# Optimization experiments

Measured on AMD Instinct MI355X. Metric: run time of the kernel, lower is better.

The kernel has to match this reference:

```python
import jax, jax.numpy as jnp
import numpy as np

B, S, D, H, N = 2, 2048, 768, 12, 128  # batch, seq_len, d_model, n_heads, num_segments
EPS_LN = 1e-5


def _layer_norm(x, g, b):
    m = x.mean(-1, keepdims=True)
    v = ((x - m) ** 2).mean(-1, keepdims=True)
    return (x - m) / jnp.sqrt(v + EPS_LN) * g + b


def _mha(q, k, v, Wqkv, bqkv, Wo, bo, n_heads):
    """torch.nn.MultiheadAttention (batch_first), returns (out, head-averaged attn)."""
    d = q.shape[-1]
    dh = d // n_heads
    Wq, Wk, Wv = jnp.split(Wqkv, 3, axis=0)
    bq, bk, bv = jnp.split(bqkv, 3)
    qh = (q @ Wq.T + bq).reshape(q.shape[0], q.shape[1], n_heads, dh)
    kh = (k @ Wk.T + bk).reshape(k.shape[0], k.shape[1], n_heads, dh)
    vh = (v @ Wv.T + bv).reshape(v.shape[0], v.shape[1], n_heads, dh)
    scores = jnp.einsum('bqhd,bkhd->bhqk', qh, kh) / jnp.sqrt(jnp.asarray(dh, q.dtype))
    attn = jax.nn.softmax(scores, axis=-1)                      # [B,H,Sq,Sk]
    out = jnp.einsum('bhqk,bkhd->bqhd', attn, vh).reshape(q.shape[0], q.shape[1], d)
    return out @ Wo.T + bo, attn.mean(axis=1)                   # attn avg over heads


def _aggregate(x, w, seg):  # per-batch: weighted mean of tokens into N segments
    num = jax.ops.segment_sum(w[:, None] * x, seg, num_segments=N)
    den = jax.ops.segment_sum(w, seg, num_segments=N)
    return num / (den[:, None] + 1e-8)


def setup_inputs() -> dict:
    key = jax.random.key(0)
    ks = jax.random.split(key, 16)
    s = 0.02
    inp = {
        'hidden_states': jax.random.normal(ks[0], (B, S, D), jnp.float32),
        'token_to_segment': jnp.sort(jax.random.randint(ks[1], (B, S), 0, N), axis=-1),
        # token_attention (shared for node-level self-attn in the adjacency=None branch)
        'Wqkv_t': jax.random.normal(ks[2], (3 * D, D), jnp.float32) * s,
        'bqkv_t': jnp.zeros((3 * D,), jnp.float32),
        'Wo_t': jax.random.normal(ks[3], (D, D), jnp.float32) * s,
        'bo_t': jnp.zeros((D,), jnp.float32),
        # cross_attention
        'Wqkv_c': jax.random.normal(ks[4], (3 * D, D), jnp.float32) * s,
        'bqkv_c': jnp.zeros((3 * D,), jnp.float32),
        'Wo_c': jax.random.normal(ks[5], (D, D), jnp.float32) * s,
        'bo_c': jnp.zeros((D,), jnp.float32),
        # layer norms
        'g_tok': jnp.ones((D,), jnp.float32),
        'b_tok': jnp.zeros((D,), jnp.float32),
        'g_node': jnp.ones((D,), jnp.float32),
        'b_node': jnp.zeros((D,), jnp.float32),
        # output projection
        'W_out': jax.random.normal(ks[6], (D, D), jnp.float32) * s,
        'b_out': jnp.zeros((D,), jnp.float32),
    }
    return inp


def reference(hidden_states, token_to_segment, Wqkv_t, bqkv_t, Wo_t, bo_t,
              Wqkv_c, bqkv_c, Wo_c, bo_c, g_tok, b_tok, g_node, b_node,
              W_out, b_out):
    hs = hidden_states
    # token-level self-attention + residual norm
    tok_attn_out, tok_attn = _mha(hs, hs, hs, Wqkv_t, bqkv_t, Wo_t, bo_t, H)
    token_output = _layer_norm(hs + tok_attn_out, g_tok, b_tok)
    # token -> node attention-weighted scatter aggregation
    w = tok_attn.mean(axis=1)  # [B,S] attention received per token
    node_emb = jax.vmap(_aggregate)(token_output, w, token_to_segment)  # [B,N,D]
    # node-level self-attention (reuses token_attention weights; adjacency=None path)
    node_out, node_attn = _mha(node_emb, node_emb, node_emb, Wqkv_t, bqkv_t, Wo_t, bo_t, H)
    node_emb = _layer_norm(node_emb + node_out, g_node, b_node)
    # cross-attention: tokens attend to nodes
    cross_out, cross_w = _mha(token_output, node_emb, node_emb, Wqkv_c, bqkv_c, Wo_c, bo_c, H)
    token_output = token_output + cross_out
    # node -> token gather + additive combine
    gathered = jnp.take_along_axis(node_emb, token_to_segment[:, :, None], axis=1)  # [B,S,D]
    enhanced = token_output + gathered
    output = enhanced @ W_out.T + b_out
    return output, node_emb, tok_attn, node_attn, cross_w
```

## Files before the change

### kernel.cpp

```cpp
#include <hip/hip_runtime.h>
#include <cstdint>

#define B_ 2
#define S_ 2048
#define D_ 768
#define H_ 12
#define DH_ 64
#define N_ 128

typedef unsigned short u16;
typedef unsigned int u32;
typedef unsigned long long u64;
typedef __attribute__((ext_vector_type(8))) short short8;
typedef __attribute__((ext_vector_type(4))) float f32x4;

#define MFMA16(a, b, c) __builtin_amdgcn_mfma_f32_16x16x32_bf16(a, b, c, 0, 0, 0)

__device__ inline u16 f2bf(float f) {
  union { float f; u32 u; } v; v.f = f;
  u32 r = v.u + 0x7FFFu + ((v.u >> 16) & 1u);
  return (u16)(r >> 16);
}
__device__ inline u32 pk2(float a, float b) {
  return (u32)f2bf(a) | ((u32)f2bf(b) << 16);
}
__device__ inline float bf2f(u16 h) {
  union { u32 u; float f; } v; v.u = ((u32)h) << 16;
  return v.f;
}
__device__ inline float wredmax(float v) {
  #pragma unroll
  for (int o = 32; o > 0; o >>= 1) v = fmaxf(v, __shfl_down(v, o));
  return v;
}
__device__ inline float wredsum(float v) {
  #pragma unroll
  for (int o = 32; o > 0; o >>= 1) v += __shfl_down(v, o);
  return v;
}
__device__ inline void async_lds16(const u16* g, u16* l) {
  __builtin_amdgcn_global_load_lds((const __attribute__((address_space(1))) void*)g,
                                   (__attribute__((address_space(3))) void*)l, 16, 0, 0);
}

__global__ void conv_bf16(const float* __restrict__ in, u16* __restrict__ outp, int n8) {
  int i = blockIdx.x * 256 + threadIdx.x;
  if (i >= n8) return;
  const float4* p = (const float4*)(in + (size_t)i * 8);
  float4 a = p[0], b = p[1];
  uint4 u;
  u.x = pk2(a.x, a.y); u.y = pk2(a.z, a.w); u.z = pk2(b.x, b.y); u.w = pk2(b.z, b.w);
  *(uint4*)(outp + (size_t)i * 8) = u;
}

template <int OUT_BF16>
__global__ __launch_bounds__(256) void gemm_bf16(
    const u16* __restrict__ A, int lda,
    const u16* __restrict__ W, int ldb,
    const float* __restrict__ bias,
    void* __restrict__ Cout, int ldc, int K) {
  __shared__ u16 As[128 * 32];
  __shared__ u16 Ws[128 * 32];
  const int tid = threadIdx.x;
  const int m0 = blockIdx.y * 128, n0 = blockIdx.x * 128;
  const int w = tid >> 6, lane = tid & 63;
  const int msub = (w & 1) * 64, nsub = (w >> 1) * 64;
  const int lrow = lane & 15, quad = lane >> 4;
  const int e0 = tid * 8;
  const int r0 = e0 >> 5, c0 = e0 & 31;
  const int e1 = e0 + 2048;
  const int r1 = e1 >> 5, c1 = e1 & 31;
  const u16* Ag0 = A + (size_t)(m0 + r0) * lda + c0;
  const u16* Ag1 = A + (size_t)(m0 + r1) * lda + c1;
  const u16* Wg0 = W + (size_t)(n0 + r0) * ldb + c0;
  const u16* Wg1 = W + (size_t)(n0 + r1) * ldb + c1;
  u16* AsB0 = As + (w << 9);
  u16* AsB1 = As + 2048 + (w << 9);
  u16* WsB0 = Ws + (w << 9);
  u16* WsB1 = Ws + 2048 + (w << 9);
  f32x4 zero = {0.f, 0.f, 0.f, 0.f};
  f32x4 acc[4][4];
  #pragma unroll
  for (int i = 0; i < 4; i++)
    #pragma unroll
    for (int j = 0; j < 4; j++) acc[i][j] = zero;
  for (int k0 = 0; k0 < K; k0 += 32) {
    __syncthreads();
    async_lds16(Ag0 + k0, AsB0);
    async_lds16(Ag1 + k0, AsB1);
    async_lds16(Wg0 + k0, WsB0);
    async_lds16(Wg1 + k0, WsB1);
    __syncthreads();
    short8 af[4], bf[4];
    #pragma unroll
    for (int i = 0; i < 4; i++)
      af[i] = *(const short8*)(As + (msub + i * 16 + lrow) * 32 + quad * 8);
    #pragma unroll
    for (int j = 0; j < 4; j++)
      bf[j] = *(const short8*)(Ws + (nsub + j * 16 + lrow) * 32 + quad * 8);
    #pragma unroll
    for (int i = 0; i < 4; i++)
      #pragma unroll
      for (int j = 0; j < 4; j++)
        acc[i][j] = MFMA16(af[i], bf[j], acc[i][j]);
  }
  #pragma unroll
  for (int i = 0; i < 4; i++) {
    #pragma unroll
    for (int j = 0; j < 4; j++) {
      int col = n0 + nsub + j * 16 + lrow;
      float bv = bias ? bias[col] : 0.f;
      #pragma unroll
      for (int r = 0; r < 4; r++) {
        int row = m0 + msub + i * 16 + quad * 4 + r;
        float val = acc[i][j][r] + bv;
        if (OUT_BF16) ((u16*)Cout)[(size_t)row * ldc + col] = f2bf(val);
        else ((float*)Cout)[(size_t)row * ldc + col] = val;
      }
    }
  }
}

__global__ __launch_bounds__(256) void transpose_v(const u16* __restrict__ qkv, u16* __restrict__ VT) {
  __shared__ u16 t[64][72];
  const int z = blockIdx.y, b = z / 12, h = z - b * 12;
  const int s0 = blockIdx.x * 64;
  const int tid = threadIdx.x;
  {
    int r = tid >> 2, dp = (tid & 3) * 16;
    const u16* src = qkv + (size_t)b * 2048 * 2304 + (size_t)(s0 + r) * 2304 + 1536 + h * 64 + dp;
    *(uint4*)&t[r][dp] = *(const uint4*)src;
    *(uint4*)&t[r][dp + 8] = *(const uint4*)(src + 8);
  }
  __syncthreads();
  int d = tid >> 2, sp = (tid & 3) * 16;
  u16 vals[16];
  #pragma unroll
  for (int i = 0; i < 16; i++) vals[i] = t[sp + i][d];
  u16* dst = VT + ((size_t)z * 64 + d) * 2048 + s0 + sp;
  *(uint4*)dst = *(uint4*)&vals[0];
  *(uint4*)(dst + 8) = *(uint4*)&vals[8];
}

__global__ __launch_bounds__(512, 4) void fused_tok_attn(
    const u16* __restrict__ qkv, const u16* __restrict__ VT,
    float* __restrict__ amF, u16* __restrict__ amH, u16* __restrict__ attnout) {
  __shared__ u16 pbuf[8][16][264];
  __shared__ float lred[8][16];
  __shared__ float obuf[2][16][66];
  const int tid = threadIdx.x;
  const int w = tid >> 6, lane = tid & 63;
  const int lrow = lane & 15, quad = lane >> 4;
  const int b = blockIdx.y, q0 = blockIdx.x << 4, z = blockIdx.z;
  const int h0 = z * 6;
  const u16* qp = qkv + (size_t)b * 2048 * 2304;
  const u16* kp = qp + 768;
  const int strip = w * 256;
  const int jj = w & 3, shalf = w >> 2;
  u16* ob = attnout + (size_t)b * 2048 * 768 + (size_t)q0 * 768;
  u16* pb = &pbuf[w][0][0];
  f32x4 zero = {0.f, 0.f, 0.f, 0.f};
  float amreg[8][8];
  #pragma unroll
  for (int c = 0; c < 8; c++)
    #pragma unroll
    for (int e = 0; e < 8; e++) amreg[c][e] = 0.f;
  for (int hh = 0; hh < 6; hh++) {
    const int h = h0 + hh;
    const u16* qh = qp + (size_t)(q0 + lrow) * 2304 + h * 64 + quad * 8;
    short8 qf0 = *(const short8*)qh;
    short8 qf1 = *(const short8*)(qh + 32);
    float lsum = 0.f;
    #pragma unroll
    for (int t = 0; t < 16; t++) {
      const u16* kh = kp + (size_t)(strip + t * 16 + lrow) * 2304 + h * 64 + quad * 8;
      short8 kf0 = *(const short8*)kh;
      short8 kf1 = *(const short8*)(kh + 32);
      f32x4 sv = zero;
      sv = MFMA16(kf0, qf0, sv);
      sv = MFMA16(kf1, qf1, sv);
      float pe0 = __expf(sv[0] * 0.125f);
      float pe1 = __expf(sv[1] * 0.125f);
      float pe2 = __expf(sv[2] * 0.125f);
      float pe3 = __expf(sv[3] * 0.125f);
      lsum += (pe0 + pe1) + (pe2 + pe3);
      u32 w0 = pk2(pe0, pe1), w1 = pk2(pe2, pe3);
      *(u64*)(pb + lrow * 264 + t * 16 + quad * 4) = (u64)w0 | ((u64)w1 << 32);
    }
    lsum += __shfl_xor(lsum, 16);
    lsum += __shfl_xor(lsum, 32);
    if (lane < 16) lred[w][lane] = lsum;
    __syncthreads();
    float invq;
    float inv4[4];
    {
      float s = 0.f;
      #pragma unroll
      for (int w2 = 0; w2 < 8; w2++) s += lred[w2][lrow];
      invq = 1.f / s;
      #pragma unroll
      for (int r = 0; r < 4; r++) {
        float sr = 0.f;
        #pragma unroll
        for (int w2 = 0; w2 < 8; w2++) sr += lred[w2][quad * 4 + r];
        inv4[r] = 1.f / sr;
      }
    }
    #pragma unroll
    for (int c = 0; c < 8; c++) {
      short8 pf = *(const short8*)(pb + lrow * 264 + c * 32 + quad * 8);
      #pragma unroll
      for (int e = 0; e < 8; e++)
        amreg[c][e] += bf2f((u16)pf[e]) * invq;
    }
    f32x4 oacc = zero;
    {
      const u16* vtp = VT + (size_t)(b * 12 + h) * 64 * 2048;
      const u16* vbase = vtp + (size_t)(jj * 16 + lrow) * 2048 + shalf * 1024 + quad * 8;
      const u16* pbase = &pbuf[shalf * 4][lrow][quad * 8];
      #pragma unroll
      for (int cc = 0; cc < 32; cc++) {
        short8 pf = *(const short8*)(pbase + (cc >> 3) * (16 * 264) + (cc & 7) * 32);
        short8 vf = *(const short8*)(vbase + cc * 32);
        oacc = MFMA16(pf, vf, oacc);
      }
    }
    #pragma unroll
    for (int r = 0; r < 4; r++)
      obuf[shalf][quad * 4 + r][jj * 16 + lrow] = oacc[r] * inv4[r];
    __syncthreads();
    #pragma unroll
    for (int ee = 0; ee < 2; ee++) {
      int e2 = tid + ee * 512;
      int row = e2 >> 6, col = e2 & 63;
      float s = obuf[0][row][col] + obuf[1][row][col];
      ob[(size_t)row * 768 + h * 64 + col] = f2bf(s);
    }
  }
  if (z == 0) {
    float* ar = amF + ((size_t)b * 2048 + q0 + lrow) * 2048 + strip;
    #pragma unroll
    for (int c = 0; c < 8; c++) {
      float4 v0 = {amreg[c][0], amreg[c][1], amreg[c][2], amreg[c][3]};
      float4 v1 = {amreg[c][4], amreg[c][5], amreg[c][6], amreg[c][7]};
      *(float4*)(ar + c * 32 + quad * 8) = v0;
      *(float4*)(ar + c * 32 + quad * 8 + 4) = v1;
    }
  } else {
    u16* ar = amH + ((size_t)b * 2048 + q0 + lrow) * 2048 + strip;
    #pragma unroll
    for (int c = 0; c < 8; c++) {
      uint4 u;
      u.x = pk2(amreg[c][0], amreg[c][1]);
      u.y = pk2(amreg[c][2], amreg[c][3]);
      u.z = pk2(amreg[c][4], amreg[c][5]);
      u.w = pk2(amreg[c][6], amreg[c][7]);
      *(uint4*)(ar + c * 32 + quad * 8) = u;
    }
  }
}

__global__ void combine_am(float* __restrict__ amF, const u16* __restrict__ amH) {
  size_t i = ((size_t)blockIdx.x * 256 + threadIdx.x) * 8;
  float4 a0 = *(float4*)(amF + i);
  float4 a1 = *(float4*)(amF + i + 4);
  uint4 hb = *(const uint4*)(amH + i);
  const float c12 = 1.f / 12.f;
  float4 r0, r1;
  r0.x = (a0.x + bf2f((u16)(hb.x & 0xffff))) * c12;
  r0.y = (a0.y + bf2f((u16)(hb.x >> 16))) * c12;
  r0.z = (a0.z + bf2f((u16)(hb.y & 0xffff))) * c12;
  r0.w = (a0.w + bf2f((u16)(hb.y >> 16))) * c12;
  r1.x = (a1.x + bf2f((u16)(hb.z & 0xffff))) * c12;
  r1.y = (a1.y + bf2f((u16)(hb.z >> 16))) * c12;
  r1.z = (a1.z + bf2f((u16)(hb.w & 0xffff))) * c12;
  r1.w = (a1.w + bf2f((u16)(hb.w >> 16))) * c12;
  *(float4*)(amF + i) = r0;
  *(float4*)(amF + i + 4) = r1;
}

__global__ __launch_bounds__(256) void qk_mfma(
    const u16* __restrict__ Q, int ldq, long qbs,
    const u16* __restrict__ Kp, int ldk, long kbs,
    float* __restrict__ S, long szs, int Sk, int nh, float scale) {
  __shared__ u16 Qs[128 * 72];
  __shared__ u16 Ks[128 * 72];
  const int tid = threadIdx.x;
  const int z = blockIdx.z, bb = z / nh, h = z - bb * nh;
  const u16* qp = Q + (size_t)bb * qbs + h * 64;
  const u16* kp = Kp + (size_t)bb * kbs + h * 64;
  float* sp = S + (size_t)z * szs;
  const int m0 = blockIdx.y * 128, n0 = blockIdx.x * 128;
  const int w = tid >> 6, lane = tid & 63;
  const int msub = (w & 1) * 64, nsub = (w >> 1) * 64;
  const int lrow = lane & 15, quad = lane >> 4;
  const int srow = tid >> 1, shalf = tid & 1;
  {
    const uint4* qg = (const uint4*)(qp + (size_t)(m0 + srow) * ldq + shalf * 32);
    const uint4* kg = (const uint4*)(kp + (size_t)(n0 + srow) * ldk + shalf * 32);
    uint4* qd = (uint4*)(Qs + srow * 72 + shalf * 32);
    uint4* kd = (uint4*)(Ks + srow * 72 + shalf * 32);
    #pragma unroll
    for (int u = 0; u < 4; u++) { qd[u] = qg[u]; kd[u] = kg[u]; }
  }
  __syncthreads();
  f32x4 zero = {0.f, 0.f, 0.f, 0.f};
  f32x4 acc[4][4];
  #pragma unroll
  for (int i = 0; i < 4; i++)
    #pragma unroll
    for (int j = 0; j < 4; j++) acc[i][j] = zero;
  #pragma unroll
  for (int ks = 0; ks < 2; ks++) {
    short8 af[4], bf[4];
    #pragma unroll
    for (int i = 0; i < 4; i++)
      af[i] = *(const short8*)(Qs + (msub + i * 16 + lrow) * 72 + ks * 32 + quad * 8);
    #pragma unroll
    for (int j = 0; j < 4; j++)
      bf[j] = *(const short8*)(Ks + (nsub + j * 16 + lrow) * 72 + ks * 32 + quad * 8);
    #pragma unroll
    for (int i = 0; i < 4; i++)
      #pragma unroll
      for (int j = 0; j < 4; j++)
        acc[i][j] = MFMA16(af[i], bf[j], acc[i][j]);
  }
  #pragma unroll
  for (int i = 0; i < 4; i++)
    #pragma unroll
    for (int j = 0; j < 4; j++) {
      int col = n0 + nsub + j * 16 + lrow;
      #pragma unroll
      for (int r = 0; r < 4; r++) {
        int row = m0 + msub + i * 16 + quad * 4 + r;
        sp[(size_t)row * Sk + col] = acc[i][j][r] * scale;
      }
    }
}

__global__ __launch_bounds__(128) void softmax_small(
    float* __restrict__ Sc, float* __restrict__ wout, int Sq) {
  const int q = blockIdx.x, b = blockIdx.y, tid = threadIdx.x;
  const int w = tid >> 6, lane = tid & 63;
  __shared__ float red[2];
  float am = 0.f;
  const size_t plane = (size_t)Sq * 128;
  for (int h = 0; h < 12; h++) {
    const int z = b * 12 + h;
    float* row = Sc + (size_t)z * plane + (size_t)q * 128;
    float v = row[tid];
    float m = wredmax(v);
    if (lane == 0) red[w] = m;
    __syncthreads();
    m = fmaxf(red[0], red[1]);
    float e = __expf(v - m);
    float s = wredsum(e);
    __syncthreads();
    if (lane == 0) red[w] = s;
    __syncthreads();
    float p = e / (red[0] + red[1]);
    ((u16*)(Sc + (size_t)z * plane))[(size_t)q * 256 + tid] = f2bf(p);
    am += p;
    __syncthreads();
  }
  wout[((size_t)b * Sq + q) * 128 + tid] = am * (1.f / 12.f);
}

__global__ __launch_bounds__(256) void pv_small(
    const u16* __restrict__ Pb, long pzs,
    const u16* __restrict__ KVb, int ldv, long vbs, int vhoff,
    u16* __restrict__ Outb, long obs) {
  __shared__ u16 Ps[128 * 40];
  __shared__ u16 Vs[64 * 40];
  const int tid = threadIdx.x;
  const int z = blockIdx.y, b = z / 12, h = z - b * 12;
  const u16* Pp = Pb + (size_t)z * pzs;
  const u16* Vp = KVb + (size_t)b * vbs + vhoff + h * 64;
  u16* Op = Outb + (size_t)b * obs + h * 64;
  const int m0 = blockIdx.x * 128;
  const int w = tid >> 6, lane = tid & 63;
  const int msub = w * 32;
  const int lrow = lane & 15, quad = lane >> 4;
  const int srow = tid >> 1, shalf = tid & 1;
  const int vk = tid >> 3, vn = (tid & 7) * 8;
  f32x4 zero = {0.f, 0.f, 0.f, 0.f};
  f32x4 acc[2][4];
  #pragma unroll
  for (int i = 0; i < 2; i++)
    #pragma unroll
    for (int j = 0; j < 4; j++) acc[i][j] = zero;
  #pragma unroll
  for (int k0 = 0; k0 < 128; k0 += 32) {
    uint4 pa = *(const uint4*)(Pp + (size_t)(m0 + srow) * 256 + k0 + shalf * 16);
    uint4 pb2 = *(const uint4*)(Pp + (size_t)(m0 + srow) * 256 + k0 + shalf * 16 + 8);
    uint4 vv = *(const uint4*)(Vp + (size_t)(k0 + vk) * ldv + vn);
    __syncthreads();
    *(uint4*)(Ps + srow * 40 + shalf * 16) = pa;
    *(uint4*)(Ps + srow * 40 + shalf * 16 + 8) = pb2;
    const u16* vs = (const u16*)&vv;
    #pragma unroll
    for (int u = 0; u < 8; u++) Vs[(vn + u) * 40 + vk] = vs[u];
    __syncthreads();
    short8 af[2], bf[4];
    #pragma unroll
    for (int i = 0; i < 2; i++)
      af[i] = *(const short8*)(Ps + (msub + i * 16 + lrow) * 40 + quad * 8);
    #pragma unroll
    for (int j = 0; j < 4; j++)
      bf[j] = *(const short8*)(Vs + (j * 16 + lrow) * 40 + quad * 8);
    #pragma unroll
    for (int i = 0; i < 2; i++)
      #pragma unroll
      for (int j = 0; j < 4; j++)
        acc[i][j] = MFMA16(af[i], bf[j], acc[i][j]);
  }
  #pragma unroll
  for (int i = 0; i < 2; i++)
    #pragma unroll
    for (int j = 0; j < 4; j++) {
      int col = j * 16 + lrow;
      #pragma unroll
      for (int r = 0; r < 4; r++) {
        int row = m0 + msub + i * 16 + quad * 4 + r;
        Op[(size_t)row * D_ + col] = f2bf(acc[i][j][r]);
      }
    }
}

__global__ void ln_kernel(const float* __restrict__ x1, const float* __restrict__ x2,
                          const float* __restrict__ g, const float* __restrict__ bt,
                          float* __restrict__ outp, u16* __restrict__ outbf) {
  const int row = blockIdx.x;
  const int tid = threadIdx.x;
  __shared__ float red[8];
  float v[3];
  #pragma unroll
  for (int j = 0; j < 3; j++) {
    int c = tid + j * 256;
    v[j] = x1[(size_t)row * D_ + c] + x2[(size_t)row * D_ + c];
  }
  float s = v[0] + v[1] + v[2];
  s = wredsum(s);
  int wid = tid >> 6, lane = tid & 63;
  if (lane == 0) red[wid] = s;
  __syncthreads();
  float mean = (red[0] + red[1] + red[2] + red[3]) / 768.f;
  float d0 = v[0] - mean, d1 = v[1] - mean, d2 = v[2] - mean;
  float q = d0 * d0 + d1 * d1 + d2 * d2;
  q = wredsum(q);
  if (lane == 0) red[4 + wid] = q;
  __syncthreads();
  float var = (red[4] + red[5] + red[6] + red[7]) / 768.f;
  float inv = rsqrtf(var + 1e-5f);
  #pragma unroll
  for (int j = 0; j < 3; j++) {
    int c = tid + j * 256;
    float val = (v[j] - mean) * inv * g[c] + bt[c];
    outp[(size_t)row * D_ + c] = val;
    if (outbf) outbf[(size_t)row * D_ + c] = f2bf(val);
  }
}

__global__ void colmean_part(const float* __restrict__ ta, float* __restrict__ part) {
  int b = blockIdx.y, z = blockIdx.z;
  int k = blockIdx.x * 256 + threadIdx.x;
  const float* p = ta + (size_t)b * S_ * S_ + (size_t)z * 256 * S_ + k;
  float s = 0.f;
  #pragma unroll 8
  for (int q = 0; q < 256; q++) s += p[(size_t)q * S_];
  part[((size_t)z * B_ + b) * S_ + k] = s;
}

__global__ void colmean_final(const float* __restrict__ part, float* __restrict__ w) {
  int b = blockIdx.y;
  int k = blockIdx.x * 256 + threadIdx.x;
  float s = 0.f;
  #pragma unroll
  for (int z = 0; z < 8; z++) s += part[((size_t)z * B_ + b) * S_ + k];
  w[b * S_ + k] = s * (1.f / (float)S_);
}

__global__ void aggregate_kernel(const float* __restrict__ x, const float* __restrict__ w,
                                 const int* __restrict__ seg, float* __restrict__ outp,
                                 u16* __restrict__ outbf) {
  const int b = blockIdx.y, n = blockIdx.x;
  const int* sg = seg + b * S_;
  int l = 0, rr = S_;
  while (l < rr) { int mid = (l + rr) >> 1; if (sg[mid] < n) l = mid + 1; else rr = mid; }
  const int lo = l;
  rr = S_;
  while (l < rr) { int mid = (l + rr) >> 1; if (sg[mid] < n + 1) l = mid + 1; else rr = mid; }
  const int hi = l;
  const int tid = threadIdx.x;
  float acc[3] = {0.f, 0.f, 0.f};
  float den = 0.f;
  for (int s = lo; s < hi; s++) {
    float ww = w[b * S_ + s];
    den += ww;
    const float* xr = x + (size_t)(b * S_ + s) * D_;
    #pragma unroll
    for (int j = 0; j < 3; j++) acc[j] += ww * xr[tid + j * 256];
  }
  float invd = 1.f / (den + 1e-8f);
  size_t ro = (size_t)(b * N_ + n) * D_;
  #pragma unroll
  for (int j = 0; j < 3; j++) {
    float val = acc[j] * invd;
    outp[ro + tid + j * 256] = val;
    outbf[ro + tid + j * 256] = f2bf(val);
  }
}

__global__ void enhanced_kernel(const float* __restrict__ tokout, const float* __restrict__ crossp,
                                const float* __restrict__ nodeemb, const int* __restrict__ seg,
                                u16* __restrict__ outbf) {
  int g8 = blockIdx.x * 256 + threadIdx.x;
  int bs = g8 / 96, d0 = (g8 - bs * 96) * 8;
  int b = bs >> 11;
  int n = seg[bs];
  const float* t = tokout + (size_t)bs * D_ + d0;
  const float* cp = crossp + (size_t)bs * D_ + d0;
  const float* ne = nodeemb + (size_t)(b * N_ + n) * D_ + d0;
  float4 a0 = *(const float4*)t, a1 = *(const float4*)(t + 4);
  float4 b0 = *(const float4*)cp, b1 = *(const float4*)(cp + 4);
  float4 c0 = *(const float4*)ne, c1 = *(const float4*)(ne + 4);
  uint4 u;
  u.x = pk2(a0.x + b0.x + c0.x, a0.y + b0.y + c0.y);
  u.y = pk2(a0.z + b0.z + c0.z, a0.w + b0.w + c0.w);
  u.z = pk2(a1.x + b1.x + c1.x, a1.y + b1.y + c1.y);
  u.w = pk2(a1.z + b1.z + c1.z, a1.w + b1.w + c1.w);
  *(uint4*)(outbf + (size_t)g8 * 8) = u;
}

extern "C" void kernel_launch(void* const* d_in, const int* in_sizes, int n_in,
                              void* d_out, int out_size, void* d_ws, size_t ws_size,
                              hipStream_t stream) {
  const float* hs     = (const float*)d_in[0];
  const int*   t2s    = (const int*)d_in[1];
  const float* Wqkv_t = (const float*)d_in[2];
  const float* bqkv_t = (const float*)d_in[3];
  const float* Wo_t   = (const float*)d_in[4];
  const float* bo_t   = (const float*)d_in[5];
  const float* Wqkv_c = (const float*)d_in[6];
  const float* bqkv_c = (const float*)d_in[7];
  const float* Wo_c   = (const float*)d_in[8];
  const float* bo_c   = (const float*)d_in[9];
  const float* g_tok  = (const float*)d_in[10];
  const float* b_tok  = (const float*)d_in[11];
  const float* g_node = (const float*)d_in[12];
  const float* b_node = (const float*)d_in[13];
  const float* W_out  = (const float*)d_in[14];
  const float* b_out  = (const float*)d_in[15];

  float* ws = (float*)d_ws;
  u16*   qkvbf       = (u16*)ws;
  u16*   enh_bf      = (u16*)ws;
  u16*   crossqbf    = (u16*)(ws + 1572864);
  u16*   crossattn_bf= (u16*)(ws + 3145728);
  float* R1 = ws + 4718592;
  u16*   hs_bf   = (u16*)R1;
  u16*   wqkvt1  = (u16*)(R1 + 1572864);
  u16*   VT      = (u16*)R1;
  u16*   amh     = (u16*)(R1 + 4194304);
  float* projbuf = R1;
  float* Snode   = R1;
  u16*   wqkvt2  = (u16*)(R1 + 4000000);
  u16*   wot     = (u16*)(R1 + 6291456);
  u16*   wqkvc   = (u16*)R1;
  u16*   woc     = (u16*)(R1 + 6291456);
  u16*   wout    = (u16*)(R1 + 6586368);
  float* Scross  = R1;
  float* crossproj = R1;
  float* R2 = ws + 13107200;
  u16*   attnout_bf = (u16*)R2;
  u16*   tokout_bf  = (u16*)R2;
  float* wvec       = R2 + 1572864;
  float* colpart    = R2 + 1576960;
  float* nodepre    = R2 + 1609728;
  float* nodeproj   = R2 + 1806336;
  u16*   nodepre_bf = (u16*)(R2 + 2002944);
  u16*   nodeattn_bf= (u16*)(R2 + 2101248);
  u16*   nodeemb_bf = (u16*)(R2 + 2199552);
  u16*   nodeqkvbf  = (u16*)(R2 + 2297856);
  u16*   crosskvbf  = (u16*)(R2 + 2592768);
  float* tokout = ws + 16252928;

  float* outp       = (float*)d_out;
  float* o_output   = outp;
  float* o_nodeemb  = outp + 3145728;
  float* o_tokattn  = o_nodeemb + 196608;
  float* o_nodeattn = o_tokattn + 8388608;
  float* o_crossw   = o_nodeattn + 32768;

  conv_bf16<<<1536, 256, 0, stream>>>(hs, hs_bf, 393216);
  conv_bf16<<<864, 256, 0, stream>>>(Wqkv_t, wqkvt1, 221184);
  gemm_bf16<1><<<dim3(18, 32), 256, 0, stream>>>(hs_bf, 768, wqkvt1, 768, bqkv_t, qkvbf, 2304, 768);

  transpose_v<<<dim3(32, 24), 256, 0, stream>>>(qkvbf, VT);
  fused_tok_attn<<<dim3(128, 2, 2), 512, 0, stream>>>(qkvbf, VT, o_tokattn, amh, attnout_bf);
  combine_am<<<4096, 256, 0, stream>>>(o_tokattn, amh);

  conv_bf16<<<288, 256, 0, stream>>>(Wo_t, wot, 73728);
  gemm_bf16<0><<<dim3(6, 32), 256, 0, stream>>>(attnout_bf, 768, wot, 768, bo_t, projbuf, 768, 768);
  ln_kernel<<<4096, 256, 0, stream>>>(hs, projbuf, g_tok, b_tok, tokout, tokout_bf);

  colmean_part<<<dim3(8, 2, 8), 256, 0, stream>>>(o_tokattn, colpart);
  colmean_final<<<dim3(8, 2), 256, 0, stream>>>(colpart, wvec);
  aggregate_kernel<<<dim3(128, 2), 256, 0, stream>>>(tokout, wvec, t2s, nodepre, nodepre_bf);
  conv_bf16<<<864, 256, 0, stream>>>(Wqkv_t, wqkvt2, 221184);
  gemm_bf16<1><<<dim3(18, 2), 256, 0, stream>>>(nodepre_bf, 768, wqkvt2, 768, bqkv_t, nodeqkvbf, 2304, 768);
  qk_mfma<<<dim3(1, 1, 24), 256, 0, stream>>>(
      nodeqkvbf, 2304, (long)128 * 2304, nodeqkvbf + 768, 2304, (long)128 * 2304,
      Snode, 16384, 128, 12, 0.125f);
  softmax_small<<<dim3(128, 2), 128, 0, stream>>>(Snode, o_nodeattn, 128);
  pv_small<<<dim3(1, 24), 256, 0, stream>>>(
      (const u16*)Snode, 32768, nodeqkvbf, 2304, (long)128 * 2304, 1536,
      nodeattn_bf, (long)128 * 768);
  gemm_bf16<0><<<dim3(6, 2), 256, 0, stream>>>(nodeattn_bf, 768, wot, 768, bo_t, nodeproj, 768, 768);
  ln_kernel<<<256, 256, 0, stream>>>(nodepre, nodeproj, g_node, b_node, o_nodeemb, nodeemb_bf);

  conv_bf16<<<864, 256, 0, stream>>>(Wqkv_c, wqkvc, 221184);
  conv_bf16<<<288, 256, 0, stream>>>(Wo_c, woc, 73728);
  conv_bf16<<<288, 256, 0, stream>>>(W_out, wout, 73728);
  gemm_bf16<1><<<dim3(6, 32), 256, 0, stream>>>(tokout_bf, 768, wqkvc, 768, bqkv_c, crossqbf, 768, 768);
  gemm_bf16<1><<<dim3(12, 2), 256, 0, stream>>>(nodeemb_bf, 768, wqkvc + 768 * 768, 768, bqkv_c + 768,
                                                crosskvbf, 1536, 768);

  qk_mfma<<<dim3(1, 16, 24), 256, 0, stream>>>(
      crossqbf, 768, (long)2048 * 768, crosskvbf, 1536, (long)128 * 1536,
      Scross, 262144, 128, 12, 0.125f);
  softmax_small<<<dim3(2048, 2), 128, 0, stream>>>(Scross, o_crossw, 2048);
  pv_small<<<dim3(16, 24), 256, 0, stream>>>(
      (const u16*)Scross, 524288, crosskvbf, 1536, (long)128 * 1536, 768,
      crossattn_bf, (long)2048 * 768);

  gemm_bf16<0><<<dim3(6, 32), 256, 0, stream>>>(crossattn_bf, 768, woc, 768, bo_c, crossproj, 768, 768);
  enhanced_kernel<<<1536, 256, 0, stream>>>(tokout, crossproj, o_nodeemb, t2s, enh_bf);
  gemm_bf16<0><<<dim3(6, 32), 256, 0, stream>>>(enh_bf, 768, wout, 768, b_out, o_output, 768, 768);
}
```

Measured before the change: 629.9 us.

## Process two query tiles per block in fused token attention with XCD-aware mapping

Each block of the fused token-attention kernel now handles 32 query rows as two 16-row groups, so every K fragment and V fragment loaded from global memory feeds two MFMAs. The launch becomes a flat 256-block grid, with the block index mapped so that blocks sharing a batch and head-half land on the same XCD, which should improve L2 reuse of K/V. The float-to-bf16 packing now uses the hardware v_cvt_pk_bf16_f32 instruction. In exchange the per-thread accumulator registers and the LDS footprint double and the occupancy hint is dropped, so there are half as many blocks and possibly lower occupancy.

```diff
diff --git a/kernel.cpp b/kernel.cpp
--- a/kernel.cpp
+++ b/kernel.cpp
@@ -23,6 +23,11 @@
 }
 __device__ inline u32 pk2(float a, float b) {
   return (u32)f2bf(a) | ((u32)f2bf(b) << 16);
+}
+__device__ inline u32 cvtpk(float lo, float hi) {
+  u32 r;
+  asm("v_cvt_pk_bf16_f32 %0, %1, %2" : "=v"(r) : "v"(lo), "v"(hi));
+  return r;
 }
 __device__ inline float bf2f(u16 h) {
   union { u32 u; float f; } v; v.u = ((u32)h) << 16;
@@ -142,120 +147,157 @@
   *(uint4*)(dst + 8) = *(uint4*)&vals[8];
 }
 
-__global__ __launch_bounds__(512, 4) void fused_tok_attn(
+__global__ __launch_bounds__(512) void fused_tok_attn(
     const u16* __restrict__ qkv, const u16* __restrict__ VT,
     float* __restrict__ amF, u16* __restrict__ amH, u16* __restrict__ attnout) {
-  __shared__ u16 pbuf[8][16][264];
-  __shared__ float lred[8][16];
-  __shared__ float obuf[2][16][66];
+  __shared__ u16 pbuf[8 * 2 * 16 * 264];
+  __shared__ float lred[8][2][16];
+  __shared__ float obuf[2][2][16][66];
   const int tid = threadIdx.x;
   const int w = tid >> 6, lane = tid & 63;
   const int lrow = lane & 15, quad = lane >> 4;
-  const int b = blockIdx.y, q0 = blockIdx.x << 4, z = blockIdx.z;
+  const int lid = blockIdx.x;
+  const int xcd = lid & 7;
+  const int combo = xcd >> 1;
+  const int b = combo >> 1, z = combo & 1;
+  const int q0 = (((lid >> 3) << 1) + (xcd & 1)) << 5;
   const int h0 = z * 6;
   const u16* qp = qkv + (size_t)b * 2048 * 2304;
   const u16* kp = qp + 768;
   const int strip = w * 256;
-  const int jj = w & 3, shalf = w >> 2;
+  const int jj = w & 3, sh = w >> 2;
   u16* ob = attnout + (size_t)b * 2048 * 768 + (size_t)q0 * 768;
-  u16* pb = &pbuf[w][0][0];
+  u16* pbA = pbuf + (w * 2 + 0) * 16 * 264;
+  u16* pbB = pbuf + (w * 2 + 1) * 16 * 264;
   f32x4 zero = {0.f, 0.f, 0.f, 0.f};
-  float amreg[8][8];
-  #pragma unroll
-  for (int c = 0; c < 8; c++)
-    #pragma unroll
-    for (int e = 0; e < 8; e++) amreg[c][e] = 0.f;
+  float amreg[2][8][8];
+  #pragma unroll
+  for (int g = 0; g < 2; g++)
+    #pragma unroll
+    for (int c = 0; c < 8; c++)
+      #pragma unroll
+      for (int e = 0; e < 8; e++) amreg[g][c][e] = 0.f;
   for (int hh = 0; hh < 6; hh++) {
     const int h = h0 + hh;
-    const u16* qh = qp + (size_t)(q0 + lrow) * 2304 + h * 64 + quad * 8;
-    short8 qf0 = *(const short8*)qh;
-    short8 qf1 = *(const short8*)(qh + 32);
-    float lsum = 0.f;
+    const u16* qhA = qp + (size_t)(q0 + lrow) * 2304 + h * 64 + quad * 8;
+    const u16* qhB = qp + (size_t)(q0 + 16 + lrow) * 2304 + h * 64 + quad * 8;
+    short8 qfA0 = *(const short8*)qhA;
+    short8 qfA1 = *(const short8*)(qhA + 32);
+    short8 qfB0 = *(const short8*)qhB;
+    short8 qfB1 = *(const short8*)(qhB + 32);
+    float lsumA = 0.f, lsumB = 0.f;
     #pragma unroll
     for (int t = 0; t < 16; t++) {
       const u16* kh = kp + (size_t)(strip + t * 16 + lrow) * 2304 + h * 64 + quad * 8;
       short8 kf0 = *(const short8*)kh;
       short8 kf1 = *(const short8*)(kh + 32);
-      f32x4 sv = zero;
-      sv = MFMA16(kf0, qf0, sv);
-      sv = MFMA16(kf1, qf1, sv);
-      float pe0 = __expf(sv[0] * 0.125f);
-      float pe1 = __expf(sv[1] * 0.125f);
-      float pe2 = __expf(sv[2] * 0.125f);
-      float pe3 = __expf(sv[3] * 0.125f);
-      lsum += (pe0 + pe1) + (pe2 + pe3);
-      u32 w0 = pk2(pe0, pe1), w1 = pk2(pe2, pe3);
-      *(u64*)(pb + lrow * 264 + t * 16 + quad * 4) = (u64)w0 | ((u64)w1 << 32);
-    }
-    lsum += __shfl_xor(lsum, 16);
-    lsum += __shfl_xor(lsum, 32);
-    if (lane < 16) lred[w][lane] = lsum;
-    __syncthreads();
-    float invq;
-    float inv4[4];
+      f32x4 svA = zero, svB = zero;
+      svA = MFMA16(kf0, qfA0, svA);
+      svA = MFMA16(kf1, qfA1, svA);
+      svB = MFMA16(kf0, qfB0, svB);
+      svB = MFMA16(kf1, qfB1, svB);
+      float a0 = __expf(svA[0] * 0.125f);
+      float a1 = __expf(svA[1] * 0.125f);
+      float a2 = __expf(svA[2] * 0.125f);
+      float a3 = __expf(svA[3] * 0.125f);
+      float b0 = __expf(svB[0] * 0.125f);
+      float b1 = __expf(svB[1] * 0.125f);
+      float b2 = __expf(svB[2] * 0.125f);
+      float b3 = __expf(svB[3] * 0.125f);
+      lsumA += (a0 + a1) + (a2 + a3);
+      lsumB += (b0 + b1) + (b2 + b3);
+      u32 wA0 = cvtpk(a0, a1), wA1 = cvtpk(a2, a3);
+      u32 wB0 = cvtpk(b0, b1), wB1 = cvtpk(b2, b3);
+      *(u64*)(pbA + lrow * 264 + t * 16 + quad * 4) = (u64)wA0 | ((u64)wA1 << 32);
+      *(u64*)(pbB + lrow * 264 + t * 16 + quad * 4) = (u64)wB0 | ((u64)wB1 << 32);
+    }
+    lsumA += __shfl_xor(lsumA, 16);
+    lsumA += __shfl_xor(lsumA, 32);
+    lsumB += __shfl_xor(lsumB, 16);
+    lsumB += __shfl_xor(lsumB, 32);
+    if (lane < 16) { lred[w][0][lane] = lsumA; lred[w][1][lane] = lsumB; }
+    __syncthreads();
+    float invqA, invqB;
+    float inv4A[4], inv4B[4];
     {
-      float s = 0.f;
-      #pragma unroll
-      for (int w2 = 0; w2 < 8; w2++) s += lred[w2][lrow];
-      invq = 1.f / s;
+      float sA = 0.f, sB = 0.f;
+      #pragma unroll
+      for (int w2 = 0; w2 < 8; w2++) { sA += lred[w2][0][lrow]; sB += lred[w2][1][lrow]; }
+      invqA = 1.f / sA; invqB = 1.f / sB;
       #pragma unroll
       for (int r = 0; r < 4; r++) {
-        float sr = 0.f;
+        float rA = 0.f, rB = 0.f;
         #pragma unroll
-        for (int w2 = 0; w2 < 8; w2++) sr += lred[w2][quad * 4 + r];
-        inv4[r] = 1.f / sr;
+        for (int w2 = 0; w2 < 8; w2++) {
+          rA += lred[w2][0][quad * 4 + r];
+          rB += lred[w2][1][quad * 4 + r];
+        }
+        inv4A[r] = 1.f / rA; inv4B[r] = 1.f / rB;
       }
     }
     #pragma unroll
     for (int c = 0; c < 8; c++) {
-      short8 pf = *(const short8*)(pb + lrow * 264 + c * 32 + quad * 8);
-      #pragma unroll
-      for (int e = 0; e < 8; e++)
-        amreg[c][e] += bf2f((u16)pf[e]) * invq;
-    }
-    f32x4 oacc = zero;
+      short8 pfa = *(const short8*)(pbA + lrow * 264 + c * 32 + quad * 8);
+      short8 pfb = *(const short8*)(pbB + lrow * 264 + c * 32 + quad * 8);
+      #pragma unroll
+      for (int e = 0; e < 8; e++) {
+        amreg[0][c][e] += bf2f((u16)pfa[e]) * invqA;
+        amreg[1][c][e] += bf2f((u16)pfb[e]) * invqB;
+      }
+    }
+    f32x4 oA = zero, oB = zero;
     {
       const u16* vtp = VT + (size_t)(b * 12 + h) * 64 * 2048;
-      const u16* vbase = vtp + (size_t)(jj * 16 + lrow) * 2048 + shalf * 1024 + quad * 8;
-      const u16* pbase = &pbuf[shalf * 4][lrow][quad * 8];
+      const u16* vbase = vtp + (size_t)(jj * 16 + lrow) * 2048 + sh * 1024 + quad * 8;
       #pragma unroll
       for (int cc = 0; cc < 32; cc++) {
-        short8 pf = *(const short8*)(pbase + (cc >> 3) * (16 * 264) + (cc & 7) * 32);
         short8 vf = *(const short8*)(vbase + cc * 32);
-        oacc = MFMA16(pf, vf, oacc);
-      }
-    }
-    #pragma unroll
-    for (int r = 0; r < 4; r++)
-      obuf[shalf][quad * 4 + r][jj * 16 + lrow] = oacc[r] * inv4[r];
-    __syncthreads();
-    #pragma unroll
-    for (int ee = 0; ee < 2; ee++) {
+        const u16* pba = pbuf + (((4 * sh + (cc >> 3)) * 2 + 0) * 16 * 264) + lrow * 264 + (cc & 7) * 32 + quad * 8;
+        const u16* pbb = pba + 16 * 264;
+        oA = MFMA16(*(const short8*)pba, vf, oA);
+        oB = MFMA16(*(const short8*)pbb, vf, oB);
+      }
+    }
+    #pragma unroll
+    for (int r = 0; r < 4; r++) {
+      obuf[0][sh][quad * 4 + r][jj * 16 + lrow] = oA[r] * inv4A[r];
+      obuf[1][sh][quad * 4 + r][jj * 16 + lrow] = oB[r] * inv4B[r];
+    }
+    __syncthreads();
+    #pragma unroll
+    for (int ee = 0; ee < 4; ee++) {
       int e2 = tid + ee * 512;
       int row = e2 >> 6, col = e2 & 63;
-      float s = obuf[0][row][col] + obuf[1][row][col];
+      int g = row >> 4, rr = row & 15;
+      float s = obuf[g][0][rr][col] + obuf[g][1][rr][col];
       ob[(size_t)row * 768 + h * 64 + col] = f2bf(s);
     }
   }
   if (z == 0) {
-    float* ar = amF + ((size_t)b * 2048 + q0 + lrow) * 2048 + strip;
-    #pragma unroll
-    for (int c = 0; c < 8; c++) {
-      float4 v0 = {amreg[c][0], amreg[c][1], amreg[c][2], amreg[c][3]};
-      float4 v1 = {amreg[c][4], amreg[c][5], amreg[c][6], amreg[c][7]};
-      *(float4*)(ar + c * 32 + quad * 8) = v0;
-      *(float4*)(ar + c * 32 + quad * 8 + 4) = v1;
+    #pragma unroll
+    for (int g = 0; g < 2; g++) {
+      float* ar = amF + ((size_t)b * 2048 + q0 + g * 16 + lrow) * 2048 + strip;
+      #pragma unroll
+      for (int c = 0; c < 8; c++) {
+        float4 v0 = {amreg[g][c][0], amreg[g][c][1], amreg[g][c][2], amreg[g][c][3]};
+        float4 v1 = {amreg[g][c][4], amreg[g][c][5], amreg[g][c][6], amreg[g][c][7]};
+        *(float4*)(ar + c * 32 + quad * 8) = v0;
+        *(float4*)(ar + c * 32 + quad * 8 + 4) = v1;
+      }
     }
   } else {
-    u16* ar = amH + ((size_t)b * 2048 + q0 + lrow) * 2048 + strip;
-    #pragma unroll
-    for (int c = 0; c < 8; c++) {
-      uint4 u;
-      u.x = pk2(amreg[c][0], amreg[c][1]);
-      u.y = pk2(amreg[c][2], amreg[c][3]);
-      u.z = pk2(amreg[c][4], amreg[c][5]);
-      u.w = pk2(amreg[c][6], amreg[c][7]);
-      *(uint4*)(ar + c * 32 + quad * 8) = u;
+    #pragma unroll
+    for (int g = 0; g < 2; g++) {
+      u16* ar = amH + ((size_t)b * 2048 + q0 + g * 16 + lrow) * 2048 + strip;
+      #pragma unroll
+      for (int c = 0; c < 8; c++) {
+        uint4 u;
+        u.x = pk2(amreg[g][c][0], amreg[g][c][1]);
+        u.y = pk2(amreg[g][c][2], amreg[g][c][3]);
+        u.z = pk2(amreg[g][c][4], amreg[g][c][5]);
+        u.w = pk2(amreg[g][c][6], amreg[g][c][7]);
+        *(uint4*)(ar + c * 32 + quad * 8) = u;
+      }
     }
   }
 }
@@ -597,7 +639,7 @@
   gemm_bf16<1><<<dim3(18, 32), 256, 0, stream>>>(hs_bf, 768, wqkvt1, 768, bqkv_t, qkvbf, 2304, 768);
 
   transpose_v<<<dim3(32, 24), 256, 0, stream>>>(qkvbf, VT);
-  fused_tok_attn<<<dim3(128, 2, 2), 512, 0, stream>>>(qkvbf, VT, o_tokattn, amh, attnout_bf);
+  fused_tok_attn<<<256, 512, 0, stream>>>(qkvbf, VT, o_tokattn, amh, attnout_bf);
   combine_am<<<4096, 256, 0, stream>>>(o_tokattn, amh);
 
   conv_bf16<<<288, 256, 0, stream>>>(Wo_t, wot, 73728);
```

Measured after the change: 556.9 us. 1.13x faster.
